# Optimization experiments

Hardware: AMD Instinct MI355X
Metric: run time of the kernel (lower is better)

## Reference

```python
import jax, jax.numpy as jnp
import numpy as np

B, S, D, H = 4, 2048, 1024, 16
HD = D // H  # head_size = 64


def setup_inputs() -> dict:
    key = jax.random.key(0)
    kx, kq, kk, kv = jax.random.split(key, 4)
    scale = 1.0 / np.sqrt(D)
    return {
        "x": jax.random.normal(kx, (B, S, D), dtype=jnp.float32),
        "Wq": jax.random.normal(kq, (H, HD, D), dtype=jnp.float32) * scale,
        "Wk": jax.random.normal(kk, (H, HD, D), dtype=jnp.float32) * scale,
        "Wv": jax.random.normal(kv, (H, HD, D), dtype=jnp.float32) * scale,
    }


def reference(x, Wq, Wk, Wv):
    # Per-head projections (Linear with weight [out, in]: y = x @ W.T),
    # vectorized over heads: [B,S,D] x [H,HD,D] -> [B,H,S,HD]
    q = jnp.einsum('bsd,hed->bhse', x, Wq)
    k = jnp.einsum('bsd,hed->bhse', x, Wk)
    v = jnp.einsum('bsd,hed->bhse', x, Wv)

    # Scaled scores: [B,H,S,S]
    att = jnp.einsum('bhqe,bhke->bhqk', q, k) / jnp.sqrt(jnp.asarray(HD, x.dtype))

    # Causal mask (lower-triangular incl. diagonal)
    causal = jnp.tril(jnp.ones((S, S), dtype=bool))
    att = jnp.where(causal, att, -jnp.inf)
    att = jax.nn.softmax(att, axis=-1)

    # Weighted values, then concat heads along feature dim -> [B,S,D]
    out = jnp.einsum('bhqk,bhke->bhqe', att, v)
    out = out.transpose(0, 2, 1, 3).reshape(B, S, H * HD)
    return out
```

## Files before the change

### kernel.cpp

```cpp
#include <hip/hip_runtime.h>
#include <hip/hip_bf16.h>

#define BATCH 4
#define S_LEN 2048
#define D_DIM 1024
#define NHEAD 16
#define HDIM 64

#define QSCALE 0.18033688011112042f

typedef __attribute__((ext_vector_type(8))) __bf16 bf16x8;
typedef __attribute__((ext_vector_type(4))) __bf16 bf16x4;
typedef __attribute__((ext_vector_type(4))) float f32x4;

static __device__ inline unsigned int bf16_bits(float f) {
    __bf16 h = (__bf16)f;
    return (unsigned int)__builtin_bit_cast(unsigned short, h);
}

__global__ __launch_bounds__(256) void cvt_kernel(
    const float* __restrict__ src, __bf16* __restrict__ dst, int n8)
{
    int i = blockIdx.x * 256 + threadIdx.x;
    if (i >= n8) return;
    const f32x4* p = reinterpret_cast<const f32x4*>(src + (size_t)i * 8);
    f32x4 a = p[0], b = p[1];
    bf16x8 r;
    r[0] = (__bf16)a[0]; r[1] = (__bf16)a[1]; r[2] = (__bf16)a[2]; r[3] = (__bf16)a[3];
    r[4] = (__bf16)b[0]; r[5] = (__bf16)b[1]; r[6] = (__bf16)b[2]; r[7] = (__bf16)b[3];
    *reinterpret_cast<bf16x8*>(dst + (size_t)i * 8) = r;
}

__global__ __launch_bounds__(256) void proj_gemm_kernel(
    const __bf16* __restrict__ xb, const __bf16* __restrict__ wb,
    __bf16* __restrict__ qo, __bf16* __restrict__ ko, __bf16* __restrict__ vto)
{
    __shared__ __bf16 As[128][32];
    __shared__ __bf16 Bs[128][32];

    const int tid = threadIdx.x;
    const int l  = tid & 63;
    const int w  = tid >> 6;
    const int wm = w >> 1, wn = w & 1;
    const int lr = l & 15, lg = l >> 4, lk = lg * 8;
    const int m0 = blockIdx.y * 128;
    const int n0 = blockIdx.x * 128;
    const int mat = n0 >> 10;
    const int nb  = n0 & 1023;

    const int sr = l >> 2;
    const int sc = (l & 3) * 8;
    const int g0 = w * 2;

    f32x4 acc[4][4] = {};

    for (int d = 0; d < D_DIM; d += 32) {
        __builtin_amdgcn_global_load_lds(
            (const __attribute__((address_space(1))) void*)(xb + (size_t)(m0 + g0 * 16 + sr) * D_DIM + d + sc),
            (__attribute__((address_space(3))) void*)(&As[g0 * 16][0]), 16, 0, 0);
        __builtin_amdgcn_global_load_lds(
            (const __attribute__((address_space(1))) void*)(xb + (size_t)(m0 + (g0 + 1) * 16 + sr) * D_DIM + d + sc),
            (__attribute__((address_space(3))) void*)(&As[(g0 + 1) * 16][0]), 16, 0, 0);
        __builtin_amdgcn_global_load_lds(
            (const __attribute__((address_space(1))) void*)(wb + (size_t)(n0 + g0 * 16 + sr) * D_DIM + d + sc),
            (__attribute__((address_space(3))) void*)(&Bs[g0 * 16][0]), 16, 0, 0);
        __builtin_amdgcn_global_load_lds(
            (const __attribute__((address_space(1))) void*)(wb + (size_t)(n0 + (g0 + 1) * 16 + sr) * D_DIM + d + sc),
            (__attribute__((address_space(3))) void*)(&Bs[(g0 + 1) * 16][0]), 16, 0, 0);
        __syncthreads();

        bf16x8 af[4], bfr[4];
        #pragma unroll
        for (int mi = 0; mi < 4; ++mi)
            af[mi] = *reinterpret_cast<const bf16x8*>(&As[wm * 64 + mi * 16 + lr][lk]);
        #pragma unroll
        for (int ni = 0; ni < 4; ++ni)
            bfr[ni] = *reinterpret_cast<const bf16x8*>(&Bs[wn * 64 + ni * 16 + lr][lk]);
        #pragma unroll
        for (int mi = 0; mi < 4; ++mi) {
            #pragma unroll
            for (int ni = 0; ni < 4; ++ni)
                acc[mi][ni] = __builtin_amdgcn_mfma_f32_16x16x32_bf16(
                    af[mi], bfr[ni], acc[mi][ni], 0, 0, 0);
        }
        __syncthreads();
    }

    const float oscale = (mat == 0) ? QSCALE : 1.0f;
    #pragma unroll
    for (int mi = 0; mi < 4; ++mi) {
        const int mrow = m0 + wm * 64 + mi * 16 + lg * 4;
        const int b = mrow >> 11;
        const int s = mrow & (S_LEN - 1);
        #pragma unroll
        for (int ni = 0; ni < 4; ++ni) {
            const int n = nb + wn * 64 + ni * 16 + lr;
            const int h = n >> 6;
            const int e = n & 63;
            if (mat == 2) {
                bf16x4 pk;
                #pragma unroll
                for (int r = 0; r < 4; ++r) pk[r] = (__bf16)acc[mi][ni][r];
                *reinterpret_cast<bf16x4*>(
                    vto + ((size_t)(b * NHEAD + h) * HDIM + e) * S_LEN + s) = pk;
            } else {
                __bf16* __restrict__ dst = (mat == 0) ? qo : ko;
                #pragma unroll
                for (int r = 0; r < 4; ++r)
                    dst[((size_t)(b * NHEAD + h) * S_LEN + (s + r)) * HDIM + e] =
                        (__bf16)(acc[mi][ni][r] * oscale);
            }
        }
    }
}

template<bool MASK>
__device__ __attribute__((always_inline)) inline void quad_compute(
    int kv0, int qbase, int lr, int lg, int lk, int swz,
    const __bf16* __restrict__ kp, const __bf16* __restrict__ vp,
    const bf16x8 (&bq0)[4], const bf16x8 (&bq1)[4],
    float (&m_acc)[4], float (&l_lane)[4], f32x4 (&acc)[4][4],
    __bf16* pl_base)
{
    bf16x8 ka0[4], ka1[4];
    #pragma unroll
    for (int c = 0; c < 4; ++c) {
        const __bf16* krow = kp + (size_t)(kv0 + c * 16 + lr) * HDIM;
        ka0[c] = *reinterpret_cast<const bf16x8*>(krow + lk);
        ka1[c] = *reinterpret_cast<const bf16x8*>(krow + 32 + lk);
    }
    bf16x8 av[2][4];
    #pragma unroll
    for (int ni = 0; ni < 4; ++ni) {
        const __bf16* vrow = vp + (size_t)(ni * 16 + lr) * S_LEN + kv0;
        av[0][ni] = *reinterpret_cast<const bf16x8*>(vrow + lk);
        av[1][ni] = *reinterpret_cast<const bf16x8*>(vrow + 32 + lk);
    }

    #pragma unroll
    for (int i = 0; i < 4; ++i) {
        __bf16* pl = pl_base + i * (16 * 64);
        f32x4 s[4];
        __builtin_amdgcn_s_setprio(1);
        #pragma unroll
        for (int c = 0; c < 4; ++c) {
            f32x4 tt = {};
            tt = __builtin_amdgcn_mfma_f32_16x16x32_bf16(ka0[c], bq0[i], tt, 0, 0, 0);
            tt = __builtin_amdgcn_mfma_f32_16x16x32_bf16(ka1[c], bq1[i], tt, 0, 0, 0);
            s[c] = tt;
        }
        __builtin_amdgcn_s_setprio(0);

        if (MASK) {
            const int qrow = qbase + i * 16 + lr;
            #pragma unroll
            for (int c = 0; c < 4; ++c)
                #pragma unroll
                for (int r = 0; r < 4; ++r)
                    if (kv0 + c * 16 + lg * 4 + r > qrow) s[c][r] = -1e30f;
        }

        float a0 = fmaxf(fmaxf(s[0][0], s[0][1]), fmaxf(s[0][2], s[0][3]));
        float a1 = fmaxf(fmaxf(s[1][0], s[1][1]), fmaxf(s[1][2], s[1][3]));
        float a2 = fmaxf(fmaxf(s[2][0], s[2][1]), fmaxf(s[2][2], s[2][3]));
        float a3 = fmaxf(fmaxf(s[3][0], s[3][1]), fmaxf(s[3][2], s[3][3]));
        float mx = fmaxf(fmaxf(a0, a1), fmaxf(a2, a3));

        if (!__all(mx - m_acc[i] <= 8.0f)) {
            mx = fmaxf(mx, __shfl_xor(mx, 16));
            mx = fmaxf(mx, __shfl_xor(mx, 32));
            const float mnew = fmaxf(m_acc[i], mx);
            const float sc = exp2f(m_acc[i] - mnew);
            l_lane[i] *= sc;
            #pragma unroll
            for (int ni = 0; ni < 4; ++ni) acc[i][ni] *= sc;
            m_acc[i] = mnew;
        }

        const float mi_ = m_acc[i];
        float psum = 0.0f;
        #pragma unroll
        for (int c = 0; c < 4; ++c) {
            const float p0 = exp2f(s[c][0] - mi_);
            const float p1 = exp2f(s[c][1] - mi_);
            const float p2 = exp2f(s[c][2] - mi_);
            const float p3 = exp2f(s[c][3] - mi_);
            psum += (p0 + p1) + (p2 + p3);
            uint2 pk;
            pk.x = bf16_bits(p0) | (bf16_bits(p1) << 16);
            pk.y = bf16_bits(p2) | (bf16_bits(p3) << 16);
            *reinterpret_cast<uint2*>(pl + lr * 64 + ((c * 16 + lg * 4) ^ swz)) = pk;
        }
        l_lane[i] += psum;
    }

    __builtin_amdgcn_s_setprio(1);
    #pragma unroll
    for (int c2 = 0; c2 < 2; ++c2) {
        #pragma unroll
        for (int i = 0; i < 4; ++i) {
            __bf16* pl = pl_base + i * (16 * 64);
            const bf16x8 pa = *reinterpret_cast<const bf16x8*>(
                pl + lr * 64 + ((c2 * 32 + lk) ^ swz));
            #pragma unroll
            for (int ni = 0; ni < 4; ++ni)
                acc[i][ni] = __builtin_amdgcn_mfma_f32_16x16x32_bf16(
                    av[c2][ni], pa, acc[i][ni], 0, 0, 0);
        }
    }
    __builtin_amdgcn_s_setprio(0);
}

__global__ __launch_bounds__(64, 2) void attn_kernel(
    const __bf16* __restrict__ q, const __bf16* __restrict__ k,
    const __bf16* __restrict__ vt, float* __restrict__ out)
{
    __shared__ __bf16 plds[4][16][64];

    const int l  = threadIdx.x;
    const int lr = l & 15;
    const int lg = l >> 4;
    const int lk = lg * 8;
    const int swz = (lr & 7) << 3;

    const int n   = blockIdx.x;
    const int xcd = n & 7;
    const int m   = n >> 3;
    const int qq  = 31 - (m >> 3);
    const int bh  = xcd * 8 + (m & 7);

    const __bf16* __restrict__ kp = k  + (size_t)bh * S_LEN * HDIM;
    const __bf16* __restrict__ vp = vt + (size_t)bh * HDIM * S_LEN;
    const int bq = bh >> 4;
    const int hq = bh & 15;

    const int qbase = qq * 64;
    const int iters = qq + 1;

    const __bf16* __restrict__ qp = q + ((size_t)bh * S_LEN + qbase) * HDIM;
    bf16x8 bq0[4], bq1[4];
    #pragma unroll
    for (int i = 0; i < 4; ++i) {
        bq0[i] = *reinterpret_cast<const bf16x8*>(qp + (size_t)(i * 16 + lr) * HDIM + lk);
        bq1[i] = *reinterpret_cast<const bf16x8*>(qp + (size_t)(i * 16 + lr) * HDIM + 32 + lk);
    }

    float m_acc[4], l_lane[4];
    f32x4 acc[4][4] = {};
    #pragma unroll
    for (int i = 0; i < 4; ++i) { m_acc[i] = -1e30f; l_lane[i] = 0.0f; }

    __bf16* pl_base = &plds[0][0][0];

    #pragma unroll 1
    for (int j = 0; j < iters - 1; ++j)
        quad_compute<false>(j * 64, qbase, lr, lg, lk, swz, kp, vp,
                            bq0, bq1, m_acc, l_lane, acc, pl_base);
    quad_compute<true>((iters - 1) * 64, qbase, lr, lg, lk, swz, kp, vp,
                       bq0, bq1, m_acc, l_lane, acc, pl_base);

    #pragma unroll
    for (int i = 0; i < 4; ++i) {
        float lt = l_lane[i];
        lt += __shfl_xor(lt, 16);
        lt += __shfl_xor(lt, 32);
        const float liv = 1.0f / lt;
        float* orow = out + (size_t)(bq * S_LEN + qbase + i * 16 + lr) * D_DIM + hq * HDIM;
        #pragma unroll
        for (int ni = 0; ni < 4; ++ni) {
            f32x4 ox;
            #pragma unroll
            for (int r = 0; r < 4; ++r) ox[r] = acc[i][ni][r] * liv;
            *reinterpret_cast<f32x4*>(orow + ni * 16 + lg * 4) = ox;
        }
    }
}

extern "C" void kernel_launch(void* const* d_in, const int* in_sizes, int n_in,
                              void* d_out, int out_size, void* d_ws, size_t ws_size,
                              hipStream_t stream)
{
    const float* x  = (const float*)d_in[0];
    const float* Wq = (const float*)d_in[1];
    const float* Wk = (const float*)d_in[2];
    const float* Wv = (const float*)d_in[3];
    float* out = (float*)d_out;

    const size_t x_elems = (size_t)BATCH * S_LEN * D_DIM;
    const size_t w_elems = (size_t)D_DIM * D_DIM;
    __bf16* xb   = (__bf16*)d_out;
    __bf16* wcat = xb + x_elems;

    const size_t per_buf = (size_t)BATCH * NHEAD * S_LEN * HDIM;
    __bf16* qb = (__bf16*)d_ws;
    __bf16* kb = qb + per_buf;
    __bf16* vb = kb + per_buf;

    cvt_kernel<<<(int)(x_elems / 8 / 256), 256, 0, stream>>>(x, xb, (int)(x_elems / 8));
    cvt_kernel<<<(int)(w_elems / 8 / 256), 256, 0, stream>>>(Wq, wcat, (int)(w_elems / 8));
    cvt_kernel<<<(int)(w_elems / 8 / 256), 256, 0, stream>>>(Wk, wcat + w_elems, (int)(w_elems / 8));
    cvt_kernel<<<(int)(w_elems / 8 / 256), 256, 0, stream>>>(Wv, wcat + 2 * w_elems, (int)(w_elems / 8));

    dim3 grid1(3 * D_DIM / 128, (BATCH * S_LEN) / 128);
    proj_gemm_kernel<<<grid1, dim3(256), 0, stream>>>(xb, wcat, qb, kb, vb);

    attn_kernel<<<dim3(2048), dim3(64), 0, stream>>>(qb, kb, vb, out);
}
```

Before: 185.9 us.

## Pair causal query tiles per block and double-buffer K fragments in registers

Each attention block now processes two query tiles, tp and 31-tp, so every block does the same total causal work and the grid shrinks to 1024 single-wave blocks. The K fragments for the next KV tile are prefetched into a second register set while the current tile is computed, which is meant to hide global load latency. Launch bounds are relaxed to one block per SIMD, allowing more registers for the extra buffer. The cost is fewer resident waves for latency hiding and higher register pressure.

```diff
diff --git a/kernel.cpp b/kernel.cpp
--- a/kernel.cpp
+++ b/kernel.cpp
@@ -114,21 +114,27 @@
     }
 }
 
+struct KFrag { bf16x8 a0[4]; bf16x8 a1[4]; };
+
+__device__ __attribute__((always_inline)) inline void load_k(
+    KFrag& kf, const __bf16* __restrict__ kp, int kv0, int lr, int lk)
+{
+    #pragma unroll
+    for (int c = 0; c < 4; ++c) {
+        const __bf16* krow = kp + (size_t)(kv0 + c * 16 + lr) * HDIM;
+        kf.a0[c] = *reinterpret_cast<const bf16x8*>(krow + lk);
+        kf.a1[c] = *reinterpret_cast<const bf16x8*>(krow + 32 + lk);
+    }
+}
+
 template<bool MASK>
 __device__ __attribute__((always_inline)) inline void quad_compute(
     int kv0, int qbase, int lr, int lg, int lk, int swz,
-    const __bf16* __restrict__ kp, const __bf16* __restrict__ vp,
+    const __bf16* __restrict__ vp, const KFrag& kf,
     const bf16x8 (&bq0)[4], const bf16x8 (&bq1)[4],
     float (&m_acc)[4], float (&l_lane)[4], f32x4 (&acc)[4][4],
     __bf16* pl_base)
 {
-    bf16x8 ka0[4], ka1[4];
-    #pragma unroll
-    for (int c = 0; c < 4; ++c) {
-        const __bf16* krow = kp + (size_t)(kv0 + c * 16 + lr) * HDIM;
-        ka0[c] = *reinterpret_cast<const bf16x8*>(krow + lk);
-        ka1[c] = *reinterpret_cast<const bf16x8*>(krow + 32 + lk);
-    }
     bf16x8 av[2][4];
     #pragma unroll
     for (int ni = 0; ni < 4; ++ni) {
@@ -145,8 +151,8 @@
         #pragma unroll
         for (int c = 0; c < 4; ++c) {
             f32x4 tt = {};
-            tt = __builtin_amdgcn_mfma_f32_16x16x32_bf16(ka0[c], bq0[i], tt, 0, 0, 0);
-            tt = __builtin_amdgcn_mfma_f32_16x16x32_bf16(ka1[c], bq1[i], tt, 0, 0, 0);
+            tt = __builtin_amdgcn_mfma_f32_16x16x32_bf16(kf.a0[c], bq0[i], tt, 0, 0, 0);
+            tt = __builtin_amdgcn_mfma_f32_16x16x32_bf16(kf.a1[c], bq1[i], tt, 0, 0, 0);
             s[c] = tt;
         }
         __builtin_amdgcn_s_setprio(0);
@@ -211,7 +217,7 @@
     __builtin_amdgcn_s_setprio(0);
 }
 
-__global__ __launch_bounds__(64, 2) void attn_kernel(
+__global__ __launch_bounds__(64, 1) void attn_kernel(
     const __bf16* __restrict__ q, const __bf16* __restrict__ k,
     const __bf16* __restrict__ vt, float* __restrict__ out)
 {
@@ -226,7 +232,7 @@
     const int n   = blockIdx.x;
     const int xcd = n & 7;
     const int m   = n >> 3;
-    const int qq  = 31 - (m >> 3);
+    const int tp  = m >> 3;
     const int bh  = xcd * 8 + (m & 7);
 
     const __bf16* __restrict__ kp = k  + (size_t)bh * S_LEN * HDIM;
@@ -234,44 +240,65 @@
     const int bq = bh >> 4;
     const int hq = bh & 15;
 
-    const int qbase = qq * 64;
-    const int iters = qq + 1;
-
-    const __bf16* __restrict__ qp = q + ((size_t)bh * S_LEN + qbase) * HDIM;
-    bf16x8 bq0[4], bq1[4];
-    #pragma unroll
-    for (int i = 0; i < 4; ++i) {
-        bq0[i] = *reinterpret_cast<const bf16x8*>(qp + (size_t)(i * 16 + lr) * HDIM + lk);
-        bq1[i] = *reinterpret_cast<const bf16x8*>(qp + (size_t)(i * 16 + lr) * HDIM + 32 + lk);
-    }
-
-    float m_acc[4], l_lane[4];
-    f32x4 acc[4][4] = {};
-    #pragma unroll
-    for (int i = 0; i < 4; ++i) { m_acc[i] = -1e30f; l_lane[i] = 0.0f; }
-
     __bf16* pl_base = &plds[0][0][0];
 
     #pragma unroll 1
-    for (int j = 0; j < iters - 1; ++j)
-        quad_compute<false>(j * 64, qbase, lr, lg, lk, swz, kp, vp,
-                            bq0, bq1, m_acc, l_lane, acc, pl_base);
-    quad_compute<true>((iters - 1) * 64, qbase, lr, lg, lk, swz, kp, vp,
-                       bq0, bq1, m_acc, l_lane, acc, pl_base);
-
-    #pragma unroll
-    for (int i = 0; i < 4; ++i) {
-        float lt = l_lane[i];
-        lt += __shfl_xor(lt, 16);
-        lt += __shfl_xor(lt, 32);
-        const float liv = 1.0f / lt;
-        float* orow = out + (size_t)(bq * S_LEN + qbase + i * 16 + lr) * D_DIM + hq * HDIM;
-        #pragma unroll
-        for (int ni = 0; ni < 4; ++ni) {
-            f32x4 ox;
-            #pragma unroll
-            for (int r = 0; r < 4; ++r) ox[r] = acc[i][ni][r] * liv;
-            *reinterpret_cast<f32x4*>(orow + ni * 16 + lg * 4) = ox;
+    for (int ph = 0; ph < 2; ++ph) {
+        const int qq    = ph ? (31 - tp) : tp;
+        const int qbase = qq * 64;
+        const int iters = qq + 1;
+
+        const __bf16* __restrict__ qp = q + ((size_t)bh * S_LEN + qbase) * HDIM;
+        bf16x8 bq0[4], bq1[4];
+        #pragma unroll
+        for (int i = 0; i < 4; ++i) {
+            bq0[i] = *reinterpret_cast<const bf16x8*>(qp + (size_t)(i * 16 + lr) * HDIM + lk);
+            bq1[i] = *reinterpret_cast<const bf16x8*>(qp + (size_t)(i * 16 + lr) * HDIM + 32 + lk);
+        }
+
+        float m_acc[4], l_lane[4];
+        f32x4 acc[4][4] = {};
+        #pragma unroll
+        for (int i = 0; i < 4; ++i) { m_acc[i] = -1e30f; l_lane[i] = 0.0f; }
+
+        KFrag kA, kB;
+        load_k(kA, kp, 0, lr, lk);
+        bool useA = true;
+
+        #pragma unroll 1
+        for (int j = 0; j < iters - 1; ++j) {
+            if (useA) {
+                load_k(kB, kp, (j + 1) * 64, lr, lk);
+                quad_compute<false>(j * 64, qbase, lr, lg, lk, swz, vp, kA,
+                                    bq0, bq1, m_acc, l_lane, acc, pl_base);
+            } else {
+                load_k(kA, kp, (j + 1) * 64, lr, lk);
+                quad_compute<false>(j * 64, qbase, lr, lg, lk, swz, vp, kB,
+                                    bq0, bq1, m_acc, l_lane, acc, pl_base);
+            }
+            useA = !useA;
+        }
+        if (useA)
+            quad_compute<true>((iters - 1) * 64, qbase, lr, lg, lk, swz, vp, kA,
+                               bq0, bq1, m_acc, l_lane, acc, pl_base);
+        else
+            quad_compute<true>((iters - 1) * 64, qbase, lr, lg, lk, swz, vp, kB,
+                               bq0, bq1, m_acc, l_lane, acc, pl_base);
+
+        #pragma unroll
+        for (int i = 0; i < 4; ++i) {
+            float lt = l_lane[i];
+            lt += __shfl_xor(lt, 16);
+            lt += __shfl_xor(lt, 32);
+            const float liv = 1.0f / lt;
+            float* orow = out + (size_t)(bq * S_LEN + qbase + i * 16 + lr) * D_DIM + hq * HDIM;
+            #pragma unroll
+            for (int ni = 0; ni < 4; ++ni) {
+                f32x4 ox;
+                #pragma unroll
+                for (int r = 0; r < 4; ++r) ox[r] = acc[i][ni][r] * liv;
+                *reinterpret_cast<f32x4*>(orow + ni * 16 + lg * 4) = ox;
+            }
         }
     }
 }
@@ -304,5 +331,5 @@
     dim3 grid1(3 * D_DIM / 128, (BATCH * S_LEN) / 128);
     proj_gemm_kernel<<<grid1, dim3(256), 0, stream>>>(xb, wcat, qb, kb, vb);
 
-    attn_kernel<<<dim3(2048), dim3(64), 0, stream>>>(qb, kb, vb, out);
-}
+    attn_kernel<<<dim3(1024), dim3(64), 0, stream>>>(qb, kb, vb, out);
+}
```

Result: no change. 184.3 us (-0.8%).

## Balance causal attention work by pairing short and long query tiles per block

Applied to the files above, without the earlier changes.

The attention kernel now processes two 32-row query tiles per block, tile tp and tile 63-tp, so every block does roughly the same amount of causal work. Before, each block handled one 64-row tile, which left some blocks with far more work than others. Halving the per-tile rows also halves register and LDS state, which may allow more blocks per CU. The cost is that each K/V block fetched is reused by only 32 query rows instead of 64, and the diagonal block is partly masked. Separately, the four fp32-to-bf16 conversion launches are merged into a single kernel.

```diff
diff --git a/kernel.cpp b/kernel.cpp
--- a/kernel.cpp
+++ b/kernel.cpp
@@ -18,17 +18,32 @@
     return (unsigned int)__builtin_bit_cast(unsigned short, h);
 }
 
-__global__ __launch_bounds__(256) void cvt_kernel(
-    const float* __restrict__ src, __bf16* __restrict__ dst, int n8)
-{
-    int i = blockIdx.x * 256 + threadIdx.x;
-    if (i >= n8) return;
-    const f32x4* p = reinterpret_cast<const f32x4*>(src + (size_t)i * 8);
+#define NX8 1048576
+#define NW8 131072
+
+__global__ __launch_bounds__(256) void cvt_all_kernel(
+    const float* __restrict__ x,  const float* __restrict__ Wq,
+    const float* __restrict__ Wk, const float* __restrict__ Wv,
+    __bf16* __restrict__ xb, __bf16* __restrict__ wcat)
+{
+    const int i = blockIdx.x * 256 + threadIdx.x;
+    const float* src;
+    __bf16* dst;
+    if (i < NX8) {
+        src = x + (size_t)i * 8;
+        dst = xb + (size_t)i * 8;
+    } else {
+        const int i2 = i - NX8;
+        const int w  = i2 >> 17;
+        src = ((w == 0) ? Wq : (w == 1) ? Wk : Wv) + (size_t)(i2 & (NW8 - 1)) * 8;
+        dst = wcat + (size_t)i2 * 8;
+    }
+    const f32x4* p = reinterpret_cast<const f32x4*>(src);
     f32x4 a = p[0], b = p[1];
     bf16x8 r;
     r[0] = (__bf16)a[0]; r[1] = (__bf16)a[1]; r[2] = (__bf16)a[2]; r[3] = (__bf16)a[3];
     r[4] = (__bf16)b[0]; r[5] = (__bf16)b[1]; r[6] = (__bf16)b[2]; r[7] = (__bf16)b[3];
-    *reinterpret_cast<bf16x8*>(dst + (size_t)i * 8) = r;
+    *reinterpret_cast<bf16x8*>(dst) = r;
 }
 
 __global__ __launch_bounds__(256) void proj_gemm_kernel(
@@ -115,11 +130,11 @@
 }
 
 template<bool MASK>
-__device__ __attribute__((always_inline)) inline void quad_compute(
+__device__ __attribute__((always_inline)) inline void duo_compute(
     int kv0, int qbase, int lr, int lg, int lk, int swz,
     const __bf16* __restrict__ kp, const __bf16* __restrict__ vp,
-    const bf16x8 (&bq0)[4], const bf16x8 (&bq1)[4],
-    float (&m_acc)[4], float (&l_lane)[4], f32x4 (&acc)[4][4],
+    const bf16x8 (&bq0)[2], const bf16x8 (&bq1)[2],
+    float (&m_acc)[2], float (&l_lane)[2], f32x4 (&acc)[2][4],
     __bf16* pl_base)
 {
     bf16x8 ka0[4], ka1[4];
@@ -138,7 +153,7 @@
     }
 
     #pragma unroll
-    for (int i = 0; i < 4; ++i) {
+    for (int i = 0; i < 2; ++i) {
         __bf16* pl = pl_base + i * (16 * 64);
         f32x4 s[4];
         __builtin_amdgcn_s_setprio(1);
@@ -198,7 +213,7 @@
     #pragma unroll
     for (int c2 = 0; c2 < 2; ++c2) {
         #pragma unroll
-        for (int i = 0; i < 4; ++i) {
+        for (int i = 0; i < 2; ++i) {
             __bf16* pl = pl_base + i * (16 * 64);
             const bf16x8 pa = *reinterpret_cast<const bf16x8*>(
                 pl + lr * 64 + ((c2 * 32 + lk) ^ swz));
@@ -215,7 +230,7 @@
     const __bf16* __restrict__ q, const __bf16* __restrict__ k,
     const __bf16* __restrict__ vt, float* __restrict__ out)
 {
-    __shared__ __bf16 plds[4][16][64];
+    __shared__ __bf16 plds[2][16][64];
 
     const int l  = threadIdx.x;
     const int lr = l & 15;
@@ -226,7 +241,7 @@
     const int n   = blockIdx.x;
     const int xcd = n & 7;
     const int m   = n >> 3;
-    const int qq  = 31 - (m >> 3);
+    const int tp  = m >> 3;
     const int bh  = xcd * 8 + (m & 7);
 
     const __bf16* __restrict__ kp = k  + (size_t)bh * S_LEN * HDIM;
@@ -234,44 +249,48 @@
     const int bq = bh >> 4;
     const int hq = bh & 15;
 
-    const int qbase = qq * 64;
-    const int iters = qq + 1;
-
-    const __bf16* __restrict__ qp = q + ((size_t)bh * S_LEN + qbase) * HDIM;
-    bf16x8 bq0[4], bq1[4];
-    #pragma unroll
-    for (int i = 0; i < 4; ++i) {
-        bq0[i] = *reinterpret_cast<const bf16x8*>(qp + (size_t)(i * 16 + lr) * HDIM + lk);
-        bq1[i] = *reinterpret_cast<const bf16x8*>(qp + (size_t)(i * 16 + lr) * HDIM + 32 + lk);
-    }
-
-    float m_acc[4], l_lane[4];
-    f32x4 acc[4][4] = {};
-    #pragma unroll
-    for (int i = 0; i < 4; ++i) { m_acc[i] = -1e30f; l_lane[i] = 0.0f; }
-
     __bf16* pl_base = &plds[0][0][0];
 
     #pragma unroll 1
-    for (int j = 0; j < iters - 1; ++j)
-        quad_compute<false>(j * 64, qbase, lr, lg, lk, swz, kp, vp,
-                            bq0, bq1, m_acc, l_lane, acc, pl_base);
-    quad_compute<true>((iters - 1) * 64, qbase, lr, lg, lk, swz, kp, vp,
-                       bq0, bq1, m_acc, l_lane, acc, pl_base);
-
-    #pragma unroll
-    for (int i = 0; i < 4; ++i) {
-        float lt = l_lane[i];
-        lt += __shfl_xor(lt, 16);
-        lt += __shfl_xor(lt, 32);
-        const float liv = 1.0f / lt;
-        float* orow = out + (size_t)(bq * S_LEN + qbase + i * 16 + lr) * D_DIM + hq * HDIM;
-        #pragma unroll
-        for (int ni = 0; ni < 4; ++ni) {
-            f32x4 ox;
-            #pragma unroll
-            for (int r = 0; r < 4; ++r) ox[r] = acc[i][ni][r] * liv;
-            *reinterpret_cast<f32x4*>(orow + ni * 16 + lg * 4) = ox;
+    for (int ph = 0; ph < 2; ++ph) {
+        const int qq    = ph ? (63 - tp) : tp;
+        const int qbase = qq * 32;
+        const int iters = (qq >> 1) + 1;
+
+        const __bf16* __restrict__ qp = q + ((size_t)bh * S_LEN + qbase) * HDIM;
+        bf16x8 bq0[2], bq1[2];
+        #pragma unroll
+        for (int i = 0; i < 2; ++i) {
+            bq0[i] = *reinterpret_cast<const bf16x8*>(qp + (size_t)(i * 16 + lr) * HDIM + lk);
+            bq1[i] = *reinterpret_cast<const bf16x8*>(qp + (size_t)(i * 16 + lr) * HDIM + 32 + lk);
+        }
+
+        float m_acc[2], l_lane[2];
+        f32x4 acc[2][4] = {};
+        #pragma unroll
+        for (int i = 0; i < 2; ++i) { m_acc[i] = -1e30f; l_lane[i] = 0.0f; }
+
+        #pragma unroll 1
+        for (int j = 0; j < iters - 1; ++j)
+            duo_compute<false>(j * 64, qbase, lr, lg, lk, swz, kp, vp,
+                               bq0, bq1, m_acc, l_lane, acc, pl_base);
+        duo_compute<true>((iters - 1) * 64, qbase, lr, lg, lk, swz, kp, vp,
+                          bq0, bq1, m_acc, l_lane, acc, pl_base);
+
+        #pragma unroll
+        for (int i = 0; i < 2; ++i) {
+            float lt = l_lane[i];
+            lt += __shfl_xor(lt, 16);
+            lt += __shfl_xor(lt, 32);
+            const float liv = 1.0f / lt;
+            float* orow = out + (size_t)(bq * S_LEN + qbase + i * 16 + lr) * D_DIM + hq * HDIM;
+            #pragma unroll
+            for (int ni = 0; ni < 4; ++ni) {
+                f32x4 ox;
+                #pragma unroll
+                for (int r = 0; r < 4; ++r) ox[r] = acc[i][ni][r] * liv;
+                *reinterpret_cast<f32x4*>(orow + ni * 16 + lg * 4) = ox;
+            }
         }
     }
 }
@@ -287,7 +306,6 @@
     float* out = (float*)d_out;
 
     const size_t x_elems = (size_t)BATCH * S_LEN * D_DIM;
-    const size_t w_elems = (size_t)D_DIM * D_DIM;
     __bf16* xb   = (__bf16*)d_out;
     __bf16* wcat = xb + x_elems;
 
@@ -296,10 +314,8 @@
     __bf16* kb = qb + per_buf;
     __bf16* vb = kb + per_buf;
 
-    cvt_kernel<<<(int)(x_elems / 8 / 256), 256, 0, stream>>>(x, xb, (int)(x_elems / 8));
-    cvt_kernel<<<(int)(w_elems / 8 / 256), 256, 0, stream>>>(Wq, wcat, (int)(w_elems / 8));
-    cvt_kernel<<<(int)(w_elems / 8 / 256), 256, 0, stream>>>(Wk, wcat + w_elems, (int)(w_elems / 8));
-    cvt_kernel<<<(int)(w_elems / 8 / 256), 256, 0, stream>>>(Wv, wcat + 2 * w_elems, (int)(w_elems / 8));
+    cvt_all_kernel<<<dim3((NX8 + 3 * NW8) / 256), dim3(256), 0, stream>>>(
+        x, Wq, Wk, Wv, xb, wcat);
 
     dim3 grid1(3 * D_DIM / 128, (BATCH * S_LEN) / 128);
     proj_gemm_kernel<<<grid1, dim3(256), 0, stream>>>(xb, wcat, qb, kb, vb);
```

Result: slower. 199.6 us (+7.4%).
